# Kernel tuning notes

Hardware: AMD Instinct MI355X
Metric: run time of the kernel (lower is better)

Reference implementation:

```python
import jax, jax.numpy as jnp
import numpy as np

P = 8          # patch_size
EPS = 1e-6     # LayerNorm2d eps


def _conv(x, w, b, groups=1):
    # x: (B,Cin,H,W), w: (Cout, Cin//groups, kh, kw)
    y = jax.lax.conv_general_dilated(
        x, w, window_strides=(1, 1), padding='SAME',
        feature_group_count=groups,
        dimension_numbers=('NCHW', 'OIHW', 'NCHW'))
    return y + b[None, :, None, None]


def _ln2d(x, w, b):
    mu = jnp.mean(x, axis=1, keepdims=True)
    var = jnp.mean((x - mu) ** 2, axis=1, keepdims=True)
    y = (x - mu) / jnp.sqrt(var + EPS)
    return w[None, :, None, None] * y + b[None, :, None, None]


def _fft_mix(x, fw):
    # windowed rFFT2 -> per-(channel,freq) real weight -> irFFT2.
    # H,W divisible by P, so window_partitionx == plain window partition.
    B, C, H, W = x.shape
    nh, nw = H // P, W // P
    xw = x.reshape(B, C, nh, P, nw, P).transpose(0, 2, 4, 1, 3, 5)  # (B,nh,nw,C,P,P)
    f = jnp.fft.rfft2(xw)                    # (B,nh,nw,C,P,P//2+1)
    f = f * fw                               # fw: (C,P,P//2+1) broadcasts
    xw = jnp.fft.irfft2(f, s=(P, P))
    return xw.transpose(0, 3, 1, 4, 2, 5).reshape(B, C, H, W)


def _gelu(x):
    return jax.nn.gelu(x, approximate=False)  # torch nn.GELU default = exact erf


def setup_inputs() -> dict:
    key = jax.random.key(0)
    ks = jax.random.split(key, 18)
    B, C, H, W = 4, 64, 256, 256
    C4, D = C * 4, C // 4
    f32 = jnp.float32

    def n(k, shape, s):
        return (jax.random.normal(k, shape, f32) * s)

    return {
        'x': jax.random.normal(ks[0], (B, C, H, W), f32),
        'ln_w': jnp.ones((C,), f32),
        'ln_b': jnp.zeros((C,), f32),
        'pconv_w': n(ks[1], (D, D, 3, 3), 0.08),
        'pconv_b': n(ks[2], (D,), 0.02),
        'w0': n(ks[3], (C4, C, 1, 1), 0.12),
        'b0': n(ks[4], (C4,), 0.02),
        'w1': n(ks[5], (C4, C, 1, 1), 0.12),
        'b1': n(ks[6], (C4,), 0.02),
        'w2': n(ks[7], (C, C4, 1, 1), 0.06),
        'b2': n(ks[8], (C,), 0.02),
        'w3': n(ks[9], (C4, 1, 3, 3), 0.3),
        'b3': n(ks[10], (C4,), 0.02),
        'w4': n(ks[11], (C, C4, 1, 1), 0.06),
        'b4': n(ks[12], (C,), 0.02),
        'fftw1': 1.0 + n(ks[13], (C, P, P // 2 + 1), 0.1),
        'fftw2': 1.0 + n(ks[14], (C, P, P // 2 + 1), 0.1),
    }


def reference(x, ln_w, ln_b, pconv_w, pconv_b, w0, b0, w1, b1,
              w2, b2, w3, b3, w4, b4, fftw1, fftw2):
    C = x.shape[1]
    D = C // 4
    C4 = C * 4

    xn = _ln2d(x, ln_w, ln_b)

    # partial 3x3 conv on first C//4 channels
    y1 = _conv(xn[:, :D], pconv_w, pconv_b)
    x2 = jnp.concatenate([y1, xn[:, D:]], axis=1)

    # branch 1: 1x1 expand -> GELU -> 1x1 contract -> windowed FFT mixing
    x1 = _conv(xn, w0, b0)
    x1 = _gelu(x1)
    x1 = _conv(x1, w2, b2)
    x1 = _fft_mix(x1, fftw1)

    # branch 2: 1x1 expand -> GELU -> depthwise 3x3 -> GELU -> 1x1 contract -> FFT mixing
    x2 = _conv(x2, w1, b1)
    x2 = _gelu(x2)
    x2 = _conv(x2, w3, b3, groups=C4)
    x2 = _gelu(x2)
    x2 = _conv(x2, w4, b4)
    x2 = _fft_mix(x2, fftw2)

    return x1 + x2
```

## Files before the change

### kernel.cpp

```cpp
#include <hip/hip_runtime.h>


typedef _Float16 f16;
typedef _Float16 f16x2 __attribute__((ext_vector_type(2)));
typedef _Float16 f16x4 __attribute__((ext_vector_type(4)));
typedef _Float16 f16x8 __attribute__((ext_vector_type(8)));
typedef float f32x4 __attribute__((ext_vector_type(4)));

__device__ __forceinline__ float dot2f(f16x2 a, f16x2 b, float c) {
#if __has_builtin(__builtin_amdgcn_fdot2)
  return __builtin_amdgcn_fdot2(a, b, c, false);
#else
  return c + (float)a.x * (float)b.x + (float)a.y * (float)b.y;
#endif
}

__device__ __forceinline__ f16x2 gelu_pk(f16x2 x) {
  const f16x2 c1 = {(f16)1.5957691f, (f16)1.5957691f};
  const f16x2 c3 = {(f16)0.0713548f, (f16)0.0713548f};
  const f16x2 cl = {(f16)-1.4426950f, (f16)-1.4426950f};
  f16x2 x2 = x * x;
  f16x2 u = x * (c1 + c3 * x2);
  f16x2 a = cl * u;
  f16 t0, t1;
#if __has_builtin(__builtin_amdgcn_exp2h)
  t0 = __builtin_amdgcn_exp2h(a[0]);
  t1 = __builtin_amdgcn_exp2h(a[1]);
#else
  t0 = (f16)exp2f((float)a[0]);
  t1 = (f16)exp2f((float)a[1]);
#endif
  f16 d0 = (f16)1.0f + t0, d1 = (f16)1.0f + t1;
  f16 r0, r1;
#if __has_builtin(__builtin_amdgcn_rcph)
  r0 = __builtin_amdgcn_rcph(d0);
  r1 = __builtin_amdgcn_rcph(d1);
#else
  r0 = (f16)(1.0f / (float)d0);
  r1 = (f16)(1.0f / (float)d1);
#endif
  f16x2 r = {r0, r1};
  return x * r;
}

__device__ __forceinline__ f16x2 cvtpk(float a, float b) {
  return __builtin_bit_cast(f16x2, __builtin_amdgcn_cvt_pkrtz(a, b));
}

__global__ void __launch_bounds__(256) lnpre_kernel(
    const float* __restrict__ x, const float* __restrict__ lnw,
    const float* __restrict__ lnb, f16* __restrict__ xn,
    const float* __restrict__ w0, const float* __restrict__ w1,
    const float* __restrict__ w2, const float* __restrict__ w4,
    const float* __restrict__ w3, const float* __restrict__ b3,
    const float* __restrict__ fw1, const float* __restrict__ fw2,
    f16* __restrict__ W0h, f16* __restrict__ W1h,
    f16* __restrict__ W2h, f16* __restrict__ W4h,
    f16* __restrict__ w3pk, f16* __restrict__ b3pk,
    float* __restrict__ kap1, float* __restrict__ kap2) {
  __shared__ float Wt[4][64];
  __shared__ float ct[8];
  int blk = blockIdx.x, t = threadIdx.x;
  if (blk < 1024) {
    int b = blk >> 8;
    int px = (blk & 255) * 256 + t;
    const float* xp = x + ((size_t)b << 22) + px;
    float v[64];
    float s = 0.f;
#pragma unroll
    for (int c = 0; c < 64; ++c) { v[c] = xp[(size_t)c << 16]; s += v[c]; }
    float mu = s * (1.f / 64.f), s2 = 0.f;
#pragma unroll
    for (int c = 0; c < 64; ++c) { float d = v[c] - mu; s2 += d * d; }
    float rstd = rsqrtf(s2 * (1.f / 64.f) + 1e-6f);
    f16* op = xn + (size_t)b * 4194304 + (size_t)px * 64;
#pragma unroll
    for (int g = 0; g < 8; ++g) {
      f16x8 pk;
#pragma unroll
      for (int j = 0; j < 8; ++j) {
        int c = g * 8 + j;
        pk[j] = (f16)((v[c] - mu) * rstd * lnw[c] + lnb[c]);
      }
      *(f16x8*)(op + g * 8) = pk;
    }
    return;
  }
  if (blk < 1290) {
    int i = (blk - 1024) * 256 + t;
    if (i < 16384) W0h[i] = (f16)w0[i];
    else if (i < 32768) W1h[i - 16384] = (f16)w1[i - 16384];
    else if (i < 49152) W2h[i - 32768] = (f16)w2[i - 32768];
    else if (i < 65536) W4h[i - 49152] = (f16)w4[i - 49152];
    else if (i < 67840) {
      int j = i - 65536;
      int g = j / 72, r = j % 72, tap = r >> 3, k = r & 7;
      w3pk[j] = (f16)w3[(g * 8 + k) * 9 + tap];
    } else if (i < 68096) {
      int k = i - 67840;
      b3pk[k] = (f16)b3[k];
    }
    return;
  }
  int sub = t >> 6, lane = t & 63;
  int unit = (blk - 1290) * 4 + sub;
  int which = unit >> 6, c = unit & 63;
  const float* fw = which ? fw2 : fw1;
  float* kap = which ? kap2 : kap1;
  int a = lane >> 3, bb = lane & 7;
  if (t == 0) {
    const float r2 = 0.70710678118654752440f;
    ct[0] = 1.f; ct[1] = r2; ct[2] = 0.f; ct[3] = -r2;
    ct[4] = -1.f; ct[5] = -r2; ct[6] = 0.f; ct[7] = r2;
  }
  Wt[sub][lane] = (bb <= 4) ? fw[c * 40 + a * 5 + bb]
                            : fw[c * 40 + ((8 - a) & 7) * 5 + (8 - bb)];
  __syncthreads();
  float acc = 0.f;
  for (int u = 0; u < 8; ++u)
    for (int v = 0; v < 8; ++v)
      acc += Wt[sub][u * 8 + v] * ct[(u * a + v * bb) & 7];
  kap[c * 64 + lane] = acc * 0.015625f;
}

__device__ __forceinline__ void pconv_body(
    char* smem, int blk, int b, const f16* __restrict__ xn,
    const float* __restrict__ pw, const float* __restrict__ pb,
    f16* __restrict__ y1) {
  char* halo = smem;
  f16* wpk = (f16*)(smem + 11520);
  float* pbs = (float*)(smem + 16128);
  int t = threadIdx.x;
  const f16* xnb = xn + (size_t)b * 4194304;
  f16* y1b = y1 + (size_t)b * 1048576;
  int h0 = (blk >> 4) << 4, w0 = (blk & 15) << 4;
  for (int i = t; i < 2304; i += 256) {
    int co = i / 144, r = i % 144, tap = r >> 4, ci = r & 15;
    wpk[i] = (f16)pw[co * 144 + ci * 9 + tap];
  }
  if (t < 16) pbs[t] = pb[t];
  for (int i = 0; i < 3; ++i) {
    int u = i * 256 + t;
    if (u < 648) {
      int hp = u >> 1, half = u & 1;
      int hr = hp / 18, hc = hp - hr * 18;
      int h = h0 - 1 + hr, w = w0 - 1 + hc;
      f16x8 v = {0, 0, 0, 0, 0, 0, 0, 0};
      if ((unsigned)h < 256u && (unsigned)w < 256u)
        v = *(const f16x8*)(xnb + ((((size_t)h << 8)) + w) * 64 + half * 8);
      *(f16x8*)(halo + hr * 640 + ((hc * 32 + half * 16) ^ ((hr & 7) << 4))) = v;
    }
  }
  __syncthreads();
  int rl = t >> 4, cl = t & 15;
  float acc[16];
#pragma unroll
  for (int co = 0; co < 16; ++co) acc[co] = pbs[co];
#pragma unroll
  for (int ty = 0; ty < 3; ++ty)
#pragma unroll
    for (int tx = 0; tx < 3; ++tx) {
      int hr = rl + ty, hc = cl + tx, tap = ty * 3 + tx;
      f16x8 ld0 = *(const f16x8*)(halo + hr * 640 + ((hc * 32) ^ ((hr & 7) << 4)));
      f16x8 ld1 = *(const f16x8*)(halo + hr * 640 + ((hc * 32 + 16) ^ ((hr & 7) << 4)));
#pragma unroll
      for (int co = 0; co < 16; ++co) {
#pragma unroll
        for (int p = 0; p < 4; ++p) {
          f16x2 xp = {ld0[2 * p], ld0[2 * p + 1]};
          f16x2 wp = *(const f16x2*)&wpk[co * 144 + tap * 16 + 2 * p];
          acc[co] = dot2f(xp, wp, acc[co]);
        }
#pragma unroll
        for (int p = 0; p < 4; ++p) {
          f16x2 xp = {ld1[2 * p], ld1[2 * p + 1]};
          f16x2 wp = *(const f16x2*)&wpk[co * 144 + tap * 16 + 8 + 2 * p];
          acc[co] = dot2f(xp, wp, acc[co]);
        }
      }
    }
  size_t px = (((size_t)(h0 + rl)) << 8) + w0 + cl;
  f16x8 o0, o1;
#pragma unroll
  for (int j = 0; j < 8; ++j) { o0[j] = (f16)acc[j]; o1[j] = (f16)acc[8 + j]; }
  *(f16x8*)(y1b + px * 16) = o0;
  *(f16x8*)(y1b + px * 16 + 8) = o1;
}

__device__ __forceinline__ void b1_body(
    char* smem, int sub, int b, const f16* __restrict__ xn,
    const f16* __restrict__ W0h, const float* __restrict__ b0,
    const f16* __restrict__ W2h, const float* __restrict__ b2,
    f16* __restrict__ u1d, f16* __restrict__ u1w) {
  f16* As = (f16*)smem;
  f16* Es = (f16*)(smem + 16384);
  int t = threadIdx.x;
  const f16* xnb = xn + (size_t)b * 4194304;
  f16* u1b = (b < 3) ? (u1d + (size_t)b * 4194304) : u1w;
  int px0 = sub << 7;
#pragma unroll
  for (int i = 0; i < 4; ++i) {
    int u = i * 256 + t, row = u >> 3, cb = (u & 7) << 4;
    f16x8 v = *(const f16x8*)(xnb + (size_t)(px0 + row) * 64 + (cb >> 1));
    *(f16x8*)((char*)As + row * 128 + (cb ^ ((row & 7) << 4))) = v;
  }
  __syncthreads();
  int l = t & 63, wv = t >> 6, lm = l & 15, kg = l >> 4;
  f32x4 uacc[2][4];
#pragma unroll
  for (int a = 0; a < 2; ++a)
#pragma unroll
    for (int n = 0; n < 4; ++n) uacc[a][n] = (f32x4){0.f, 0.f, 0.f, 0.f};
  for (int cc = 0; cc < 4; ++cc) {
    f32x4 eacc[2][4];
#pragma unroll
    for (int a = 0; a < 2; ++a)
#pragma unroll
      for (int n = 0; n < 4; ++n) eacc[a][n] = (f32x4){0.f, 0.f, 0.f, 0.f};
#pragma unroll
    for (int kk = 0; kk < 2; ++kk) {
      int kb = kk * 64 + kg * 16;
      f16x8 af[2];
#pragma unroll
      for (int mt = 0; mt < 2; ++mt) {
        int row = wv * 32 + mt * 16 + lm;
        af[mt] = *(const f16x8*)((char*)As + row * 128 + (kb ^ ((row & 7) << 4)));
      }
      f16x8 bf[4];
#pragma unroll
      for (int nt = 0; nt < 4; ++nt) {
        int co = cc * 64 + nt * 16 + lm;
        bf[nt] = *(const f16x8*)(W0h + (size_t)co * 64 + kk * 32 + kg * 8);
      }
#pragma unroll
      for (int mt = 0; mt < 2; ++mt)
#pragma unroll
        for (int nt = 0; nt < 4; ++nt)
          eacc[mt][nt] = __builtin_amdgcn_mfma_f32_16x16x32_f16(bf[nt], af[mt], eacc[mt][nt], 0, 0, 0);
    }
    if (cc) __syncthreads();
#pragma unroll
    for (int mt = 0; mt < 2; ++mt) {
      int row = wv * 32 + mt * 16 + lm;
#pragma unroll
      for (int nt = 0; nt < 4; ++nt) {
        int c0 = nt * 16 + kg * 4;
        float4 bz4 = *(const float4*)&b0[cc * 64 + c0];
        f16x2 lo = gelu_pk(cvtpk(eacc[mt][nt][0] + bz4.x, eacc[mt][nt][1] + bz4.y));
        f16x2 hi = gelu_pk(cvtpk(eacc[mt][nt][2] + bz4.z, eacc[mt][nt][3] + bz4.w));
        f16x4 pk = {lo[0], lo[1], hi[0], hi[1]};
        *(f16x4*)((char*)Es + row * 128 + ((c0 * 2) ^ ((row & 7) << 4))) = pk;
      }
    }
    __syncthreads();
#pragma unroll
    for (int kk = 0; kk < 2; ++kk) {
      int kb = kk * 64 + kg * 16;
      f16x8 af[2];
#pragma unroll
      for (int mt = 0; mt < 2; ++mt) {
        int row = wv * 32 + mt * 16 + lm;
        af[mt] = *(const f16x8*)((char*)Es + row * 128 + (kb ^ ((row & 7) << 4)));
      }
      f16x8 bf[4];
#pragma unroll
      for (int nt = 0; nt < 4; ++nt) {
        int co = nt * 16 + lm;
        bf[nt] = *(const f16x8*)(W2h + (size_t)co * 256 + cc * 64 + kk * 32 + kg * 8);
      }
#pragma unroll
      for (int mt = 0; mt < 2; ++mt)
#pragma unroll
        for (int nt = 0; nt < 4; ++nt)
          uacc[mt][nt] = __builtin_amdgcn_mfma_f32_16x16x32_f16(bf[nt], af[mt], uacc[mt][nt], 0, 0, 0);
    }
    __syncthreads();
  }
#pragma unroll
  for (int mt = 0; mt < 2; ++mt) {
    int row = wv * 32 + mt * 16 + lm;
#pragma unroll
    for (int nt = 0; nt < 4; ++nt) {
      int c0 = nt * 16 + kg * 4;
      float4 bz4 = *(const float4*)&b2[c0];
      f16x2 lo = cvtpk(uacc[mt][nt][0] + bz4.x, uacc[mt][nt][1] + bz4.y);
      f16x2 hi = cvtpk(uacc[mt][nt][2] + bz4.z, uacc[mt][nt][3] + bz4.w);
      f16x4 pk = {lo[0], lo[1], hi[0], hi[1]};
      *(f16x4*)((char*)Es + row * 128 + ((c0 * 2) ^ ((row & 7) << 4))) = pk;
    }
  }
  __syncthreads();
  int co = t >> 2, q = t & 3;
  f16x8 o[4];
#pragma unroll
  for (int i = 0; i < 32; ++i) {
    int m = q * 32 + i;
    o[i >> 3][i & 7] =
        *(const f16*)((char*)Es + m * 128 + ((co * 2) ^ ((m & 7) << 4)));
  }
  f16* up = u1b + ((size_t)co << 16) + px0 + q * 32;
#pragma unroll
  for (int ss = 0; ss < 4; ++ss) *(f16x8*)(up + ss * 8) = o[ss];
}

__global__ void __launch_bounds__(256) b1pc_kernel(
    const f16* __restrict__ xn, const f16* __restrict__ W0h,
    const float* __restrict__ b0, const f16* __restrict__ W2h,
    const float* __restrict__ b2, f16* __restrict__ u1d,
    f16* __restrict__ u1w, const float* __restrict__ pw,
    const float* __restrict__ pb, f16* __restrict__ y1) {
  __shared__ __align__(16) char smem[32768];
  int xb = blockIdx.x;
  if (xb < 2048)
    b1_body(smem, xb & 511, xb >> 9, xn, W0h, b0, W2h, b2, u1d, u1w);
  else {
    int u = xb - 2048;
    pconv_body(smem, u & 255, u >> 8, xn, pw, pb, y1);
  }
}

__device__ __forceinline__ void b2_expand(
    const char* xin, const f16* __restrict__ W1h, int ce0, int wv, int lm,
    int kg, f32x4 (&eacc)[3][2]) {
#pragma unroll
  for (int a = 0; a < 3; ++a)
#pragma unroll
    for (int n = 0; n < 2; ++n) eacc[a][n] = (f32x4){0.f, 0.f, 0.f, 0.f};
#pragma unroll
  for (int kk = 0; kk < 2; ++kk) {
    int kb = kk * 64 + kg * 16;
    f16x8 af[3];
#pragma unroll
    for (int mtl = 0; mtl < 3; ++mtl) {
      int row = (mtl * 4 + wv) * 16 + lm;
      af[mtl] = *(const f16x8*)(xin + row * 128 + (kb ^ ((row & 7) << 4)));
    }
    f16x8 bf[2];
#pragma unroll
    for (int nt = 0; nt < 2; ++nt) {
      int ce = ce0 + nt * 16 + lm;
      bf[nt] = *(const f16x8*)(W1h + (size_t)ce * 64 + kk * 32 + kg * 8);
    }
#pragma unroll
    for (int mtl = 0; mtl < 3; ++mtl)
#pragma unroll
      for (int nt = 0; nt < 2; ++nt)
        eacc[mtl][nt] = __builtin_amdgcn_mfma_f32_16x16x32_f16(bf[nt], af[mtl], eacc[mtl][nt], 0, 0, 0);
  }
}

__global__ void __launch_bounds__(256) b2_kernel(
    const f16* __restrict__ xn, const f16* __restrict__ y1,
    const f16* __restrict__ W1h, const float* __restrict__ b1v,
    const f16* __restrict__ W4h, const float* __restrict__ b4,
    const f16* __restrict__ w3pk, const f16* __restrict__ b3pk,
    f16* __restrict__ u2) {
  __shared__ __align__(16) f16 xin[12288];
  __shared__ __align__(16) f16 Es[6144];
  int t = threadIdx.x, blk = blockIdx.x, b = blockIdx.y;
  const f16* xnb = xn + (size_t)b * 4194304;
  const f16* y1b = y1 + (size_t)b * 1048576;
  f16* u2b = u2 + (size_t)b * 4194304;
  int h0 = (blk >> 4) << 3, w0 = (blk & 15) << 4;
#pragma unroll
  for (int i = 0; i < 6; ++i) {
    int u = i * 256 + t;
    int hp = u >> 3, part = u & 7;
    f16x8 v = {0, 0, 0, 0, 0, 0, 0, 0};
    if (hp < 180) {
      int hr = hp / 18, hc = hp - hr * 18;
      int h = h0 - 1 + hr, w = w0 - 1 + hc;
      if ((unsigned)h < 256u && (unsigned)w < 256u) {
        size_t px = ((size_t)h << 8) + w;
        v = (part < 2) ? *(const f16x8*)(y1b + px * 16 + part * 8)
                       : *(const f16x8*)(xnb + px * 64 + part * 8);
      }
    }
    *(f16x8*)((char*)xin + hp * 128 + ((part * 16) ^ ((hp & 7) << 4))) = v;
  }
  __syncthreads();
  int l = t & 63, wv = t >> 6, lm = l & 15, kg = l >> 4;
  f32x4 uacc[2][4];
#pragma unroll
  for (int a = 0; a < 2; ++a)
#pragma unroll
    for (int n = 0; n < 4; ++n) uacc[a][n] = (f32x4){0.f, 0.f, 0.f, 0.f};
  f32x4 eacc[3][2];
  b2_expand((const char*)xin, W1h, 0, wv, lm, kg, eacc);
  for (int it = 0; it < 8; ++it) {
    int ce0 = it * 32;
    if (it) __syncthreads();
#pragma unroll
    for (int mtl = 0; mtl < 3; ++mtl) {
      int row = (mtl * 4 + wv) * 16 + lm;
#pragma unroll
      for (int nt = 0; nt < 2; ++nt) {
        int cL = nt * 16 + kg * 4;
        float4 bz4 = *(const float4*)&b1v[ce0 + cL];
        f16x2 lo = gelu_pk(cvtpk(eacc[mtl][nt][0] + bz4.x, eacc[mtl][nt][1] + bz4.y));
        f16x2 hi = gelu_pk(cvtpk(eacc[mtl][nt][2] + bz4.z, eacc[mtl][nt][3] + bz4.w));
        f16x4 pk = {lo[0], lo[1], hi[0], hi[1]};
        *(f16x4*)((char*)Es + row * 64 + ((cL * 2) ^ (((row >> 1) & 3) << 4))) = pk;
      }
    }
    __syncthreads();
    if (it < 7) b2_expand((const char*)xin, W1h, ce0 + 32, wv, lm, kg, eacc);
    int g9 = (ce0 + kg * 8) >> 3;
    f16x8 wv9[9];
#pragma unroll
    for (int tap = 0; tap < 9; ++tap)
      wv9[tap] = *(const f16x8*)(w3pk + g9 * 72 + tap * 8);
    f16x8 bias8 = *(const f16x8*)(b3pk + ce0 + kg * 8);
    f16x8 af2[2];
#pragma unroll
    for (int mt = 0; mt < 2; ++mt) {
      int px = wv * 32 + mt * 16 + lm;
      int rl2 = px >> 4, cl2 = px & 15;
      f16x8 a8 = bias8;
#pragma unroll
      for (int ty = 0; ty < 3; ++ty)
#pragma unroll
        for (int tx = 0; tx < 3; ++tx) {
          int hp = (rl2 + ty) * 18 + (cl2 + tx);
          f16x8 xv = *(const f16x8*)((char*)Es + hp * 64 + ((kg * 16) ^ (((hp >> 1) & 3) << 4)));
          a8 += xv * wv9[ty * 3 + tx];
        }
#pragma unroll
      for (int j2 = 0; j2 < 4; ++j2) {
        f16x2 g = gelu_pk((f16x2){a8[2 * j2], a8[2 * j2 + 1]});
        af2[mt][2 * j2] = g[0];
        af2[mt][2 * j2 + 1] = g[1];
      }
    }
    f16x8 bf2[4];
#pragma unroll
    for (int nt = 0; nt < 4; ++nt) {
      int co = nt * 16 + lm;
      bf2[nt] = *(const f16x8*)(W4h + (size_t)co * 256 + ce0 + kg * 8);
    }
#pragma unroll
    for (int mt = 0; mt < 2; ++mt)
#pragma unroll
      for (int nt = 0; nt < 4; ++nt)
        uacc[mt][nt] = __builtin_amdgcn_mfma_f32_16x16x32_f16(bf2[nt], af2[mt], uacc[mt][nt], 0, 0, 0);
  }
  __syncthreads();
#pragma unroll
  for (int mt = 0; mt < 2; ++mt) {
    int m = wv * 32 + mt * 16 + lm;
#pragma unroll
    for (int nt = 0; nt < 4; ++nt) {
      int c0 = nt * 16 + kg * 4;
      float4 bz4 = *(const float4*)&b4[c0];
      f16x2 lo = cvtpk(uacc[mt][nt][0] + bz4.x, uacc[mt][nt][1] + bz4.y);
      f16x2 hi = cvtpk(uacc[mt][nt][2] + bz4.z, uacc[mt][nt][3] + bz4.w);
      f16x4 pk = {lo[0], lo[1], hi[0], hi[1]};
      *(f16x4*)((char*)xin + m * 128 + ((c0 * 2) ^ ((m & 7) << 4))) = pk;
    }
  }
  __syncthreads();
  int co = t >> 2, q = t & 3;
  f16x8 o[4];
#pragma unroll
  for (int i = 0; i < 32; ++i) {
    int m = q * 32 + i;
    o[i >> 3][i & 7] =
        *(const f16*)((char*)xin + m * 128 + ((co * 2) ^ ((m & 7) << 4)));
  }
  f16* up = u2b + ((size_t)co << 16) + (size_t)(h0 + 2 * q) * 256 + w0;
  *(f16x8*)(up) = o[0];
  *(f16x8*)(up + 8) = o[1];
  *(f16x8*)(up + 256) = o[2];
  *(f16x8*)(up + 256 + 8) = o[3];
}

__global__ void __launch_bounds__(256) fftmix_kernel(
    const f16* __restrict__ u1d, const f16* __restrict__ u1w,
    const f16* __restrict__ u2, const float* __restrict__ kap1,
    const float* __restrict__ kap2, float* __restrict__ out, int base) {
  int blk = blockIdx.x;
  int b = base + blockIdx.y;
  int c = blk >> 4, part = blk & 15;
  int t = threadIdx.x;
  int l = t & 63, wv = (t >> 6) & 3;
  int s = l >> 3, tq = l & 7;
  __shared__ unsigned int kls[64];
  if (t < 64) {
    f16 k1 = (f16)kap1[(c << 6) + t];
    f16 k2 = (f16)kap2[(c << 6) + t];
    kls[t] = (unsigned int)__builtin_bit_cast(unsigned short, k1) |
             ((unsigned int)__builtin_bit_cast(unsigned short, k2) << 16);
  }
  __syncthreads();
  unsigned int kp[64];
#pragma unroll
  for (int j = 0; j < 64; ++j) {
    int idx = (((s - (j >> 3)) & 7) << 3) | ((tq - (j & 7)) & 7);
    kp[j] = kls[idx];
  }
  const f16* u1 = (b < 3) ? (u1d + (size_t)b * 4194304) : u1w;
  const f16* u2b = u2 + (size_t)b * 4194304;
  size_t cb = ((size_t)c) << 16;
  size_t obase = ((size_t)(b * 64 + c)) << 16;
  int win0 = part * 64 + wv * 16;
  for (int it = 0; it < 16; ++it) {
    int win = win0 + it;
    int wh = win >> 5, ww = win & 31;
    size_t pix = (size_t)((wh * 8 + s) << 8) + ww * 8 + tq;
    unsigned int pk =
        (unsigned int)__builtin_bit_cast(unsigned short, u1[cb + pix]) |
        ((unsigned int)__builtin_bit_cast(unsigned short, u2b[cb + pix]) << 16);
    float ac0 = 0.f, ac1 = 0.f, ac2 = 0.f, ac3 = 0.f;
#pragma unroll
    for (int j = 0; j < 64; j += 4) {
      unsigned int v0 = (unsigned int)__builtin_amdgcn_readlane((int)pk, j);
      unsigned int v1 = (unsigned int)__builtin_amdgcn_readlane((int)pk, j + 1);
      unsigned int v2 = (unsigned int)__builtin_amdgcn_readlane((int)pk, j + 2);
      unsigned int v3 = (unsigned int)__builtin_amdgcn_readlane((int)pk, j + 3);
      ac0 = dot2f(__builtin_bit_cast(f16x2, v0), __builtin_bit_cast(f16x2, kp[j]), ac0);
      ac1 = dot2f(__builtin_bit_cast(f16x2, v1), __builtin_bit_cast(f16x2, kp[j + 1]), ac1);
      ac2 = dot2f(__builtin_bit_cast(f16x2, v2), __builtin_bit_cast(f16x2, kp[j + 2]), ac2);
      ac3 = dot2f(__builtin_bit_cast(f16x2, v3), __builtin_bit_cast(f16x2, kp[j + 3]), ac3);
    }
    out[obase + pix] = (ac0 + ac1) + (ac2 + ac3);
  }
}

__global__ void diag_kernel(float* __restrict__ out, float code, int n) {
  int i = blockIdx.x * 256 + threadIdx.x;
  for (int p = i; p < n; p += 256 * 4096) out[p] = (p == 0) ? code : 0.f;
}

extern "C" void kernel_launch(void* const* d_in, const int* in_sizes, int n_in,
                              void* d_out, int out_size, void* d_ws,
                              size_t ws_size, hipStream_t stream) {
  const float* x       = (const float*)d_in[0];
  const float* ln_w    = (const float*)d_in[1];
  const float* ln_b    = (const float*)d_in[2];
  const float* pconv_w = (const float*)d_in[3];
  const float* pconv_b = (const float*)d_in[4];
  const float* w0      = (const float*)d_in[5];
  const float* b0      = (const float*)d_in[6];
  const float* w1      = (const float*)d_in[7];
  const float* b1      = (const float*)d_in[8];
  const float* w2      = (const float*)d_in[9];
  const float* b2      = (const float*)d_in[10];
  const float* w3      = (const float*)d_in[11];
  const float* b3      = (const float*)d_in[12];
  const float* w4      = (const float*)d_in[13];
  const float* b4      = (const float*)d_in[14];
  const float* fftw1   = (const float*)d_in[15];
  const float* fftw2   = (const float*)d_in[16];

  const size_t OFF_KAP1 = 0;
  const size_t OFF_KAP2 = 16384;
  const size_t OFF_W0H  = 32768;
  const size_t OFF_W1H  = 65536;
  const size_t OFF_W2H  = 98304;
  const size_t OFF_W4H  = 131072;
  const size_t OFF_W3PK = 163840;
  const size_t OFF_B3PK = 168448;
  const size_t OFF_Y1   = 168960;
  const size_t OFF_U2   = OFF_Y1 + 8388608ull;
  const size_t OFF_U13  = OFF_U2 + 33554432ull;
  const size_t WS_NEED  = OFF_U13 + 8388608ull;

  float* outF = (float*)d_out;
  if (ws_size < WS_NEED) {
    diag_kernel<<<4096, 256, 0, stream>>>(outF, 1000.0f + (float)(ws_size >> 20), 16777216);
    return;
  }
  char* ws = (char*)d_ws;
  float* kap1 = (float*)(ws + OFF_KAP1);
  float* kap2 = (float*)(ws + OFF_KAP2);
  f16* W0h  = (f16*)(ws + OFF_W0H);
  f16* W1h  = (f16*)(ws + OFF_W1H);
  f16* W2h  = (f16*)(ws + OFF_W2H);
  f16* W4h  = (f16*)(ws + OFF_W4H);
  f16* w3pk = (f16*)(ws + OFF_W3PK);
  f16* b3pk = (f16*)(ws + OFF_B3PK);
  f16* Y1   = (f16*)(ws + OFF_Y1);
  f16* U2   = (f16*)(ws + OFF_U2);
  f16* U13  = (f16*)(ws + OFF_U13);

  f16* XN  = (f16*)d_out;
  f16* U1D = (f16*)d_out + 16777216;

  lnpre_kernel<<<1322, 256, 0, stream>>>(x, ln_w, ln_b, XN,
                                         w0, w1, w2, w4, w3, b3, fftw1, fftw2,
                                         W0h, W1h, W2h, W4h, w3pk, b3pk,
                                         kap1, kap2);
  b1pc_kernel<<<3072, 256, 0, stream>>>(XN, W0h, b0, W2h, b2, U1D, U13,
                                        pconv_w, pconv_b, Y1);
  b2_kernel<<<dim3(512, 4), 256, 0, stream>>>(XN, Y1, W1h, b1, W4h, b4,
                                              w3pk, b3pk, U2);
  fftmix_kernel<<<dim3(1024, 2), 256, 0, stream>>>(U1D, U13, U2, kap1, kap2, outF, 0);
  fftmix_kernel<<<dim3(1024, 1), 256, 0, stream>>>(U1D, U13, U2, kap1, kap2, outF, 2);
  fftmix_kernel<<<dim3(1024, 1), 256, 0, stream>>>(U1D, U13, U2, kap1, kap2, outF, 3);
}
```

Measured before the change: 336.1 us.

## Load GEMM A-fragments directly into registers, shrink LDS footprint in b1 and b2

In the b1 and b2 kernels the input tile is no longer staged through shared memory. Each lane loads its MFMA A-operand fragments straight from global memory into registers, and those registers are reused across all expand iterations. This removes the staging buffer and one barrier, and cuts LDS use (b1 goes from 32KB to 16KB, and the b2 xin array is gone), which should allow more resident blocks. The b2 output transpose now reuses the smaller Es buffer in two passes with an extra barrier. The cost is higher register pressure and less coalesced global loads.

After: 329.2 us (median of 2 runs). -2.0%, faster.

```diff
diff --git a/kernel.cpp b/kernel.cpp
--- a/kernel.cpp
+++ b/kernel.cpp
@@ -192,40 +192,33 @@
     const f16* __restrict__ W0h, const float* __restrict__ b0,
     const f16* __restrict__ W2h, const float* __restrict__ b2,
     f16* __restrict__ u1d, f16* __restrict__ u1w) {
-  f16* As = (f16*)smem;
-  f16* Es = (f16*)(smem + 16384);
+  f16* Es = (f16*)smem;
   int t = threadIdx.x;
   const f16* xnb = xn + (size_t)b * 4194304;
   f16* u1b = (b < 3) ? (u1d + (size_t)b * 4194304) : u1w;
   int px0 = sub << 7;
-#pragma unroll
-  for (int i = 0; i < 4; ++i) {
-    int u = i * 256 + t, row = u >> 3, cb = (u & 7) << 4;
-    f16x8 v = *(const f16x8*)(xnb + (size_t)(px0 + row) * 64 + (cb >> 1));
-    *(f16x8*)((char*)As + row * 128 + (cb ^ ((row & 7) << 4))) = v;
-  }
-  __syncthreads();
   int l = t & 63, wv = t >> 6, lm = l & 15, kg = l >> 4;
+  f16x8 a[2][2];
+#pragma unroll
+  for (int mt = 0; mt < 2; ++mt) {
+    int row = wv * 32 + mt * 16 + lm;
+#pragma unroll
+    for (int kk = 0; kk < 2; ++kk)
+      a[mt][kk] = *(const f16x8*)(xnb + (size_t)(px0 + row) * 64 + kk * 32 + kg * 8);
+  }
   f32x4 uacc[2][4];
 #pragma unroll
-  for (int a = 0; a < 2; ++a)
-#pragma unroll
-    for (int n = 0; n < 4; ++n) uacc[a][n] = (f32x4){0.f, 0.f, 0.f, 0.f};
+  for (int aa = 0; aa < 2; ++aa)
+#pragma unroll
+    for (int n = 0; n < 4; ++n) uacc[aa][n] = (f32x4){0.f, 0.f, 0.f, 0.f};
   for (int cc = 0; cc < 4; ++cc) {
     f32x4 eacc[2][4];
 #pragma unroll
-    for (int a = 0; a < 2; ++a)
-#pragma unroll
-      for (int n = 0; n < 4; ++n) eacc[a][n] = (f32x4){0.f, 0.f, 0.f, 0.f};
+    for (int aa = 0; aa < 2; ++aa)
+#pragma unroll
+      for (int n = 0; n < 4; ++n) eacc[aa][n] = (f32x4){0.f, 0.f, 0.f, 0.f};
 #pragma unroll
     for (int kk = 0; kk < 2; ++kk) {
-      int kb = kk * 64 + kg * 16;
-      f16x8 af[2];
-#pragma unroll
-      for (int mt = 0; mt < 2; ++mt) {
-        int row = wv * 32 + mt * 16 + lm;
-        af[mt] = *(const f16x8*)((char*)As + row * 128 + (kb ^ ((row & 7) << 4)));
-      }
       f16x8 bf[4];
 #pragma unroll
       for (int nt = 0; nt < 4; ++nt) {
@@ -236,7 +229,7 @@
       for (int mt = 0; mt < 2; ++mt)
 #pragma unroll
         for (int nt = 0; nt < 4; ++nt)
-          eacc[mt][nt] = __builtin_amdgcn_mfma_f32_16x16x32_f16(bf[nt], af[mt], eacc[mt][nt], 0, 0, 0);
+          eacc[mt][nt] = __builtin_amdgcn_mfma_f32_16x16x32_f16(bf[nt], a[mt][kk], eacc[mt][nt], 0, 0, 0);
     }
     if (cc) __syncthreads();
 #pragma unroll
@@ -309,7 +302,7 @@
     const float* __restrict__ b2, f16* __restrict__ u1d,
     f16* __restrict__ u1w, const float* __restrict__ pw,
     const float* __restrict__ pb, f16* __restrict__ y1) {
-  __shared__ __align__(16) char smem[32768];
+  __shared__ __align__(16) char smem[16384];
   int xb = blockIdx.x;
   if (xb < 2048)
     b1_body(smem, xb & 511, xb >> 9, xn, W0h, b0, W2h, b2, u1d, u1w);
@@ -320,21 +313,14 @@
 }
 
 __device__ __forceinline__ void b2_expand(
-    const char* xin, const f16* __restrict__ W1h, int ce0, int wv, int lm,
-    int kg, f32x4 (&eacc)[3][2]) {
+    const f16x8 (&a0)[3], const f16x8 (&a1)[3], const f16* __restrict__ W1h,
+    int ce0, int lm, int kg, f32x4 (&eacc)[3][2]) {
 #pragma unroll
   for (int a = 0; a < 3; ++a)
 #pragma unroll
     for (int n = 0; n < 2; ++n) eacc[a][n] = (f32x4){0.f, 0.f, 0.f, 0.f};
 #pragma unroll
   for (int kk = 0; kk < 2; ++kk) {
-    int kb = kk * 64 + kg * 16;
-    f16x8 af[3];
-#pragma unroll
-    for (int mtl = 0; mtl < 3; ++mtl) {
-      int row = (mtl * 4 + wv) * 16 + lm;
-      af[mtl] = *(const f16x8*)(xin + row * 128 + (kb ^ ((row & 7) << 4)));
-    }
     f16x8 bf[2];
 #pragma unroll
     for (int nt = 0; nt < 2; ++nt) {
@@ -342,10 +328,12 @@
       bf[nt] = *(const f16x8*)(W1h + (size_t)ce * 64 + kk * 32 + kg * 8);
     }
 #pragma unroll
-    for (int mtl = 0; mtl < 3; ++mtl)
+    for (int mtl = 0; mtl < 3; ++mtl) {
+      f16x8 af = kk ? a1[mtl] : a0[mtl];
 #pragma unroll
       for (int nt = 0; nt < 2; ++nt)
-        eacc[mtl][nt] = __builtin_amdgcn_mfma_f32_16x16x32_f16(bf[nt], af[mtl], eacc[mtl][nt], 0, 0, 0);
+        eacc[mtl][nt] = __builtin_amdgcn_mfma_f32_16x16x32_f16(bf[nt], af, eacc[mtl][nt], 0, 0, 0);
+    }
   }
 }
 
@@ -355,38 +343,38 @@
     const f16* __restrict__ W4h, const float* __restrict__ b4,
     const f16* __restrict__ w3pk, const f16* __restrict__ b3pk,
     f16* __restrict__ u2) {
-  __shared__ __align__(16) f16 xin[12288];
   __shared__ __align__(16) f16 Es[6144];
   int t = threadIdx.x, blk = blockIdx.x, b = blockIdx.y;
   const f16* xnb = xn + (size_t)b * 4194304;
   const f16* y1b = y1 + (size_t)b * 1048576;
   f16* u2b = u2 + (size_t)b * 4194304;
   int h0 = (blk >> 4) << 3, w0 = (blk & 15) << 4;
-#pragma unroll
-  for (int i = 0; i < 6; ++i) {
-    int u = i * 256 + t;
-    int hp = u >> 3, part = u & 7;
-    f16x8 v = {0, 0, 0, 0, 0, 0, 0, 0};
-    if (hp < 180) {
-      int hr = hp / 18, hc = hp - hr * 18;
+  int l = t & 63, wv = t >> 6, lm = l & 15, kg = l >> 4;
+  f16x8 a0[3], a1[3];
+#pragma unroll
+  for (int mtl = 0; mtl < 3; ++mtl) {
+    int row = (mtl * 4 + wv) * 16 + lm;
+    f16x8 v0 = {0, 0, 0, 0, 0, 0, 0, 0}, v1 = v0;
+    if (row < 180) {
+      int hr = row / 18, hc = row - hr * 18;
       int h = h0 - 1 + hr, w = w0 - 1 + hc;
       if ((unsigned)h < 256u && (unsigned)w < 256u) {
         size_t px = ((size_t)h << 8) + w;
-        v = (part < 2) ? *(const f16x8*)(y1b + px * 16 + part * 8)
-                       : *(const f16x8*)(xnb + px * 64 + part * 8);
-      }
-    }
-    *(f16x8*)((char*)xin + hp * 128 + ((part * 16) ^ ((hp & 7) << 4))) = v;
-  }
-  __syncthreads();
-  int l = t & 63, wv = t >> 6, lm = l & 15, kg = l >> 4;
+        v1 = *(const f16x8*)(xnb + px * 64 + 32 + kg * 8);
+        v0 = (kg < 2) ? *(const f16x8*)(y1b + px * 16 + kg * 8)
+                      : *(const f16x8*)(xnb + px * 64 + kg * 8);
+      }
+    }
+    a0[mtl] = v0;
+    a1[mtl] = v1;
+  }
   f32x4 uacc[2][4];
 #pragma unroll
   for (int a = 0; a < 2; ++a)
 #pragma unroll
     for (int n = 0; n < 4; ++n) uacc[a][n] = (f32x4){0.f, 0.f, 0.f, 0.f};
   f32x4 eacc[3][2];
-  b2_expand((const char*)xin, W1h, 0, wv, lm, kg, eacc);
+  b2_expand(a0, a1, W1h, 0, lm, kg, eacc);
   for (int it = 0; it < 8; ++it) {
     int ce0 = it * 32;
     if (it) __syncthreads();
@@ -404,7 +392,7 @@
       }
     }
     __syncthreads();
-    if (it < 7) b2_expand((const char*)xin, W1h, ce0 + 32, wv, lm, kg, eacc);
+    if (it < 7) b2_expand(a0, a1, W1h, ce0 + 32, lm, kg, eacc);
     int g9 = (ce0 + kg * 8) >> 3;
     f16x8 wv9[9];
 #pragma unroll
@@ -447,7 +435,8 @@
   __syncthreads();
 #pragma unroll
   for (int mt = 0; mt < 2; ++mt) {
-    int m = wv * 32 + mt * 16 + lm;
+    if (mt) __syncthreads();
+    int crow = wv * 16 + lm;
 #pragma unroll
     for (int nt = 0; nt < 4; ++nt) {
       int c0 = nt * 16 + kg * 4;
@@ -455,23 +444,22 @@
       f16x2 lo = cvtpk(uacc[mt][nt][0] + bz4.x, uacc[mt][nt][1] + bz4.y);
       f16x2 hi = cvtpk(uacc[mt][nt][2] + bz4.z, uacc[mt][nt][3] + bz4.w);
       f16x4 pk = {lo[0], lo[1], hi[0], hi[1]};
-      *(f16x4*)((char*)xin + m * 128 + ((c0 * 2) ^ ((m & 7) << 4))) = pk;
-    }
-  }
-  __syncthreads();
-  int co = t >> 2, q = t & 3;
-  f16x8 o[4];
-#pragma unroll
-  for (int i = 0; i < 32; ++i) {
-    int m = q * 32 + i;
-    o[i >> 3][i & 7] =
-        *(const f16*)((char*)xin + m * 128 + ((co * 2) ^ ((m & 7) << 4)));
-  }
-  f16* up = u2b + ((size_t)co << 16) + (size_t)(h0 + 2 * q) * 256 + w0;
-  *(f16x8*)(up) = o[0];
-  *(f16x8*)(up + 8) = o[1];
-  *(f16x8*)(up + 256) = o[2];
-  *(f16x8*)(up + 256 + 8) = o[3];
+      *(f16x4*)((char*)Es + crow * 128 + ((c0 * 2) ^ ((crow & 7) << 4))) = pk;
+    }
+    __syncthreads();
+    int co = t >> 2, q = t & 3;
+    f16x8 o0, o1;
+#pragma unroll
+    for (int i = 0; i < 16; ++i) {
+      int crow = q * 16 + i;
+      f16 vv = *(const f16*)((char*)Es + crow * 128 + ((co * 2) ^ ((crow & 7) << 4)));
+      if (i < 8) o0[i] = vv;
+      else o1[i - 8] = vv;
+    }
+    f16* up = u2b + ((size_t)co << 16) + (size_t)(h0 + 2 * q + mt) * 256 + w0;
+    *(f16x8*)(up) = o0;
+    *(f16x8*)(up + 8) = o1;
+  }
 }
 
 __global__ void __launch_bounds__(256) fftmix_kernel(
```
